# Performance work log

Hardware: AMD Instinct MI355X
Metric: run time of the kernel (lower is better)

## Reference

```python
import jax, jax.numpy as jnp
import numpy as np
import math

B, S, D, H, DQ = 4, 1024, 1024, 16, 64
DV = DQ // 2  # per-head value dim (all_head_size/2 split over heads)
MASK_VAL = -10000.0


def setup_inputs() -> dict:
    key = jax.random.key(0)
    ks = jax.random.split(key, 9)
    s = 1.0 / math.sqrt(D)
    return {
        "input_matrix": jax.random.normal(ks[0], (B, S, D), jnp.float32),
        "Wq": jax.random.normal(ks[1], (D, H * DQ), jnp.float32) * s,
        "bq": jnp.zeros((H * DQ,), jnp.float32),
        "Wk": jax.random.normal(ks[2], (D, H * DQ), jnp.float32) * s,
        "bk": jnp.zeros((H * DQ,), jnp.float32),
        "Wv": jax.random.normal(ks[3], (D, H * DV), jnp.float32) * s,
        "bv": jnp.zeros((H * DV,), jnp.float32),
        "Wo": jax.random.normal(ks[4], (D, D), jnp.float32) * s,
        "bo": jnp.zeros((D,), jnp.float32),
    }


def reference(input_matrix, Wq, bq, Wk, bk, Wv, bv, Wo, bo):
    x = input_matrix
    # projections -> [B, H, S, d]
    q = (x @ Wq + bq).reshape(B, S, H, DQ).transpose(0, 2, 1, 3)
    k = (x @ Wk + bk).reshape(B, S, H, DQ).transpose(0, 2, 1, 3)
    v = (x @ Wv + bv).reshape(B, S, H, DV).transpose(0, 2, 1, 3)

    scores = jnp.einsum("bhqd,bhkd->bhqk", q, k) / math.sqrt(DQ)  # [B,H,S,S]

    tril = jnp.tril(jnp.ones((S, S), bool))  # causal keep-mask
    fwd_scores = jnp.where(tril, scores, MASK_VAL)      # look-ahead masking
    bwd_scores = jnp.where(tril.T, scores, MASK_VAL)    # look-behind masking

    fwd_prob = jax.nn.softmax(fwd_scores, axis=-1)
    bwd_prob = jax.nn.softmax(bwd_scores, axis=-1)

    fwd_out = jnp.einsum("bhqk,bhkd->bhqd", fwd_prob, v)
    bwd_out = jnp.einsum("bhqk,bhkd->bhqd", bwd_prob, v)
    # [B,H,S,DV] -> [B,S,H*DV]
    fwd_out = fwd_out.transpose(0, 2, 1, 3).reshape(B, S, H * DV)
    bwd_out = bwd_out.transpose(0, 2, 1, 3).reshape(B, S, H * DV)

    out = jnp.concatenate([fwd_out, bwd_out], axis=-1) @ Wo + bo  # [B,S,D]
    attn_prob = jnp.concatenate([fwd_prob, bwd_prob], axis=-1)    # [B,H,S,2S]
    return out, attn_prob
```

## Files before the change

kernel.cpp:

```cpp
#include <hip/hip_runtime.h>
#include <hip/hip_bf16.h>

#define S_ 1024
#define D_ 1024
#define H_ 16
#define DQ_ 64
#define DV_ 32

typedef __attribute__((ext_vector_type(8))) short bf16x8;
typedef __attribute__((ext_vector_type(4))) float f32x4;

static __device__ __forceinline__ float bf2f(unsigned short u) {
    union { unsigned int i; float f; } v; v.i = ((unsigned int)u) << 16; return v.f;
}
static __device__ __forceinline__ unsigned short f2bf(float f) {
    union { float f; unsigned int i; } v; v.f = f;
    unsigned int x = v.i;
    unsigned int r = x + 0x7fffu + ((x >> 16) & 1u);
    return (unsigned short)(r >> 16);
}
static __device__ __forceinline__ f32x4 mfma16(bf16x8 a, bf16x8 b, f32x4 c) {
    return __builtin_amdgcn_mfma_f32_16x16x32_bf16(a, b, c, 0, 0, 0);
}

static __device__ __forceinline__ void gload16(const unsigned short* g, unsigned short* l) {
    __builtin_amdgcn_global_load_lds(
        (const __attribute__((address_space(1))) unsigned int*)(unsigned long long)g,
        (__attribute__((address_space(3))) unsigned int*)(unsigned int)(unsigned long long)l,
        16, 0, 0);
}

__global__ void k_detect(const unsigned short* __restrict__ X, int* __restrict__ flag) {
    int tid = threadIdx.x;
    unsigned short u = X[2 * tid];
    int e = (u >> 7) & 0xFF;
    bool sane = (e >= 100 && e <= 150) || ((u & 0x7FFFu) == 0);
    unsigned long long m = __ballot(sane);
    if (tid == 0) *flag = (__popcll(m) >= 40) ? 1 : 0;
}

__global__ void k_cvt(const void* __restrict__ src, unsigned short* __restrict__ dst,
                      int n, const int* __restrict__ flag) {
    int i = blockIdx.x * 256 + threadIdx.x;
    if (i >= n) return;
    int fl = *flag;
    dst[i] = fl ? ((const unsigned short*)src)[i] : f2bf(((const float*)src)[i]);
}

__global__ void k_cvt_f(const void* __restrict__ src, float* __restrict__ dst,
                        int n, const int* __restrict__ flag) {
    int i = blockIdx.x * 256 + threadIdx.x;
    if (i >= n) return;
    int fl = *flag;
    dst[i] = fl ? bf2f(((const unsigned short*)src)[i]) : ((const float*)src)[i];
}

__global__ void k_transpose(const void* __restrict__ src,
                            unsigned short* __restrict__ dst, int K, int N,
                            const int* __restrict__ flag) {
    __shared__ unsigned short t[32][33];
    int fl = *flag;
    int n0 = blockIdx.x * 32, k0 = blockIdx.y * 32;
    int tx = threadIdx.x, ty = threadIdx.y;
    for (int i = ty; i < 32; i += 8) {
        size_t idx = (size_t)(k0 + i) * N + n0 + tx;
        t[i][tx] = fl ? ((const unsigned short*)src)[idx]
                      : f2bf(((const float*)src)[idx]);
    }
    __syncthreads();
    for (int i = ty; i < 32; i += 8)
        dst[(size_t)(n0 + i) * K + k0 + tx] = t[tx][i];
}

__global__ __launch_bounds__(256)
void k_qkv(const unsigned short* __restrict__ Xb,
           const unsigned short* __restrict__ WT,
           const float* __restrict__ bias_f,
           unsigned short* __restrict__ q_l,
           unsigned short* __restrict__ k_l,
           unsigned short* __restrict__ vT) {
    __shared__ __align__(16) unsigned short As[128 * 32];
    __shared__ __align__(16) unsigned short Bs[128 * 32];
    int tid = threadIdx.x;
    int w = tid >> 6, lane = tid & 63;
    int m = lane & 15, quad = lane >> 4;
    int row0 = blockIdx.y * 128;
    int col0 = blockIdx.x * 128;
    int wr = w >> 1, wc = w & 1;

    const unsigned short* a0 = Xb + (size_t)(row0 + (tid >> 2)) * 1024 + (tid & 3) * 8;
    const unsigned short* b0 = WT + (size_t)(col0 + (tid >> 2)) * 1024 + (tid & 3) * 8;
    unsigned short* AsW = As + w * 512;
    unsigned short* BsW = Bs + w * 512;

    f32x4 acc[4][4];
#pragma unroll
    for (int i = 0; i < 4; ++i)
#pragma unroll
        for (int j = 0; j < 4; ++j) acc[i][j] = (f32x4){0.f, 0.f, 0.f, 0.f};

    for (int k0 = 0; k0 < 1024; k0 += 32) {
        gload16(a0 + k0, AsW);
        gload16(a0 + 64 * 1024 + k0, AsW + 2048);
        gload16(b0 + k0, BsW);
        gload16(b0 + 64 * 1024 + k0, BsW + 2048);
        __syncthreads();
        bf16x8 af[4], bf[4];
#pragma unroll
        for (int f = 0; f < 4; ++f) {
            af[f] = *(const bf16x8*)&As[(wr * 64 + f * 16 + m) * 32 + quad * 8];
            bf[f] = *(const bf16x8*)&Bs[(wc * 64 + f * 16 + m) * 32 + quad * 8];
        }
#pragma unroll
        for (int i = 0; i < 4; ++i)
#pragma unroll
            for (int j = 0; j < 4; ++j)
                acc[i][j] = mfma16(af[i], bf[j], acc[i][j]);
        __syncthreads();
    }

#pragma unroll
    for (int fn = 0; fn < 4; ++fn) {
        int col = col0 + wc * 64 + fn * 16 + m;
        float bval = bias_f[col];
#pragma unroll
        for (int fm = 0; fm < 4; ++fm) {
#pragma unroll
            for (int j = 0; j < 4; ++j) {
                int row = row0 + wr * 64 + fm * 16 + quad * 4 + j;
                int bb = row >> 10, ss = row & 1023;
                unsigned short o = f2bf(acc[fm][fn][j] + bval);
                if (col < 1024) {
                    int h = col >> 6, d = col & 63;
                    q_l[(((size_t)(bb * H_ + h)) * S_ + ss) * DQ_ + d] = o;
                } else if (col < 2048) {
                    int c = col - 1024; int h = c >> 6, d = c & 63;
                    k_l[(((size_t)(bb * H_ + h)) * S_ + ss) * DQ_ + d] = o;
                } else {
                    int c = col - 2048; int h = c >> 5, dv = c & 31;
                    vT[(((size_t)(bb * H_ + h)) * DV_ + dv) * S_ + ss] = o;
                }
            }
        }
    }
}

__global__ __launch_bounds__(256)
void k_attn(const unsigned short* __restrict__ q_l,
            const unsigned short* __restrict__ k_l,
            const unsigned short* __restrict__ vT,
            unsigned short* __restrict__ probs_b,
            float* __restrict__ probs_f,
            unsigned short* __restrict__ Y,
            const int* __restrict__ flag) {
    __shared__ __align__(16) unsigned short P[2][16][1032];
    __shared__ float redM[4][2][16];
    __shared__ float redL[4][2][16];
    int fl = *flag;
    int tid = threadIdx.x;
    int w = tid >> 6, lane = tid & 63;
    int m = lane & 15, quad = lane >> 4;
    int bh = blockIdx.x;
    int q0 = blockIdx.y * 16;
    int kbase = w * 256;

    const unsigned short* qp = q_l + (size_t)bh * S_ * DQ_;
    const unsigned short* kp = k_l + (size_t)bh * S_ * DQ_;
    const unsigned short* vp = vT  + (size_t)bh * DV_ * S_;

    bf16x8 qa0 = *(const bf16x8*)(qp + (size_t)(q0 + m) * DQ_ + quad * 8);
    bf16x8 qa1 = *(const bf16x8*)(qp + (size_t)(q0 + m) * DQ_ + 32 + quad * 8);

    float sc[16][4];
#pragma unroll
    for (int t = 0; t < 16; ++t) {
        const unsigned short* krow = kp + (size_t)((kbase >> 4) * 16 + t * 16 + m) * DQ_;
        bf16x8 kb0 = *(const bf16x8*)(krow + quad * 8);
        bf16x8 kb1 = *(const bf16x8*)(krow + 32 + quad * 8);
        f32x4 s = {0.f, 0.f, 0.f, 0.f};
        s = mfma16(qa0, kb0, s);
        s = mfma16(qa1, kb1, s);
#pragma unroll
        for (int j = 0; j < 4; ++j) sc[t][j] = s[j] * 0.125f;
    }

#pragma unroll
    for (int j = 0; j < 4; ++j) {
        int row = quad * 4 + j;
        int r = q0 + row;
        float mF = -3e38f, mB = -3e38f;
#pragma unroll
        for (int t = 0; t < 16; ++t) {
            int c = kbase + t * 16 + m;
            float v = sc[t][j];
            mF = (c <= r) ? fmaxf(mF, v) : mF;
            mB = (c >= r) ? fmaxf(mB, v) : mB;
        }
        mF = fmaxf(mF, __shfl_xor(mF, 1, 64));
        mF = fmaxf(mF, __shfl_xor(mF, 2, 64));
        mF = fmaxf(mF, __shfl_xor(mF, 4, 64));
        mF = fmaxf(mF, __shfl_xor(mF, 8, 64));
        mB = fmaxf(mB, __shfl_xor(mB, 1, 64));
        mB = fmaxf(mB, __shfl_xor(mB, 2, 64));
        mB = fmaxf(mB, __shfl_xor(mB, 4, 64));
        mB = fmaxf(mB, __shfl_xor(mB, 8, 64));
        if (m == 0) { redM[w][0][row] = mF; redM[w][1][row] = mB; }
    }
    __syncthreads();

#pragma unroll
    for (int j = 0; j < 4; ++j) {
        int row = quad * 4 + j;
        int r = q0 + row;
        float gmF = fmaxf(fmaxf(redM[0][0][row], redM[1][0][row]),
                          fmaxf(redM[2][0][row], redM[3][0][row]));
        float gmB = fmaxf(fmaxf(redM[0][1][row], redM[1][1][row]),
                          fmaxf(redM[2][1][row], redM[3][1][row]));
        float corr = __expf(gmF - gmB);
        float sF = 0.f, sB = 0.f;
#pragma unroll
        for (int t = 0; t < 16; ++t) {
            int c = kbase + t * 16 + m;
            float v = sc[t][j];
            bool fwd = (c <= r);
            float e = __expf(v - (fwd ? gmF : gmB));
            float eF = fwd ? e : 0.f;
            float eB = (c > r) ? e : ((c == r) ? e * corr : 0.f);
            sF += eF; sB += eB;
            P[0][row][c] = f2bf(eF);
            P[1][row][c] = f2bf(eB);
        }
        sF += __shfl_xor(sF, 1, 64);
        sF += __shfl_xor(sF, 2, 64);
        sF += __shfl_xor(sF, 4, 64);
        sF += __shfl_xor(sF, 8, 64);
        sB += __shfl_xor(sB, 1, 64);
        sB += __shfl_xor(sB, 2, 64);
        sB += __shfl_xor(sB, 4, 64);
        sB += __shfl_xor(sB, 8, 64);
        if (m == 0) { redL[w][0][row] = sF; redL[w][1][row] = sB; }
    }
    __syncthreads();

    size_t pbase = (size_t)bh << 21;
#pragma unroll 4
    for (int i = 0; i < 32; ++i) {
        int row = i >> 1, dir = i & 1;
        int col4 = tid * 4;
        ushort4 ev = *(const ushort4*)&P[dir][row][col4];
        float l = redL[0][dir][row] + redL[1][dir][row] +
                  redL[2][dir][row] + redL[3][dir][row];
        float inv = 1.f / l;
        size_t off = pbase + (size_t)(q0 + row) * 2048 + (size_t)dir * 1024 + col4;
        if (fl) {
            ushort4 o;
            o.x = f2bf(bf2f(ev.x) * inv); o.y = f2bf(bf2f(ev.y) * inv);
            o.z = f2bf(bf2f(ev.z) * inv); o.w = f2bf(bf2f(ev.w) * inv);
            *(ushort4*)(probs_b + off) = o;
        } else {
            float4 o = { bf2f(ev.x) * inv, bf2f(ev.y) * inv,
                         bf2f(ev.z) * inv, bf2f(ev.w) * inv };
            *(float4*)(probs_f + off) = o;
        }
    }

    {
        int dir = w >> 1, half = w & 1;
        const unsigned short* vrow = vp + (size_t)(half * 16 + m) * S_;
        f32x4 acc0 = {0.f,0.f,0.f,0.f}, acc1 = {0.f,0.f,0.f,0.f};
#pragma unroll
        for (int it = 0; it < 32; it += 2) {
            bf16x8 a0 = *(const bf16x8*)&P[dir][m][it * 32 + quad * 8];
            bf16x8 b0 = *(const bf16x8*)(vrow + it * 32 + quad * 8);
            acc0 = mfma16(a0, b0, acc0);
            bf16x8 a1 = *(const bf16x8*)&P[dir][m][it * 32 + 32 + quad * 8];
            bf16x8 b1 = *(const bf16x8*)(vrow + it * 32 + 32 + quad * 8);
            acc1 = mfma16(a1, b1, acc1);
        }
        int b_ = bh >> 4, h_ = bh & 15;
#pragma unroll
        for (int j = 0; j < 4; ++j) {
            int row = quad * 4 + j;
            float l = redL[0][dir][row] + redL[1][dir][row] +
                      redL[2][dir][row] + redL[3][dir][row];
            float v = (acc0[j] + acc1[j]) / l;
            Y[((size_t)(b_ * 1024 + q0 + row)) * 1024 +
              dir * 512 + h_ * 32 + half * 16 + m] = f2bf(v);
        }
    }
}

__global__ __launch_bounds__(256)
void k_out(const unsigned short* __restrict__ Y,
           const unsigned short* __restrict__ WoT,
           const float* __restrict__ bo,
           unsigned short* __restrict__ out_b,
           float* __restrict__ out_f,
           const int* __restrict__ flag) {
    __shared__ __align__(16) unsigned short As[128 * 32];
    __shared__ __align__(16) unsigned short Bs[128 * 32];
    int fl = *flag;
    int tid = threadIdx.x;
    int w = tid >> 6, lane = tid & 63;
    int m = lane & 15, quad = lane >> 4;
    int row0 = blockIdx.y * 128;
    int col0 = blockIdx.x * 128;
    int wr = w >> 1, wc = w & 1;

    const unsigned short* a0 = Y   + (size_t)(row0 + (tid >> 2)) * 1024 + (tid & 3) * 8;
    const unsigned short* b0 = WoT + (size_t)(col0 + (tid >> 2)) * 1024 + (tid & 3) * 8;
    unsigned short* AsW = As + w * 512;
    unsigned short* BsW = Bs + w * 512;

    f32x4 acc[4][4];
#pragma unroll
    for (int i = 0; i < 4; ++i)
#pragma unroll
        for (int j = 0; j < 4; ++j) acc[i][j] = (f32x4){0.f, 0.f, 0.f, 0.f};

    for (int k0 = 0; k0 < 1024; k0 += 32) {
        gload16(a0 + k0, AsW);
        gload16(a0 + 64 * 1024 + k0, AsW + 2048);
        gload16(b0 + k0, BsW);
        gload16(b0 + 64 * 1024 + k0, BsW + 2048);
        __syncthreads();
        bf16x8 af[4], bf[4];
#pragma unroll
        for (int f = 0; f < 4; ++f) {
            af[f] = *(const bf16x8*)&As[(wr * 64 + f * 16 + m) * 32 + quad * 8];
            bf[f] = *(const bf16x8*)&Bs[(wc * 64 + f * 16 + m) * 32 + quad * 8];
        }
#pragma unroll
        for (int i = 0; i < 4; ++i)
#pragma unroll
            for (int j = 0; j < 4; ++j)
                acc[i][j] = mfma16(af[i], bf[j], acc[i][j]);
        __syncthreads();
    }

#pragma unroll
    for (int fn = 0; fn < 4; ++fn) {
        int col = col0 + wc * 64 + fn * 16 + m;
        float bval = bo[col];
#pragma unroll
        for (int fm = 0; fm < 4; ++fm) {
#pragma unroll
            for (int j = 0; j < 4; ++j) {
                int row = row0 + wr * 64 + fm * 16 + quad * 4 + j;
                float v = acc[fm][fn][j] + bval;
                if (fl) out_b[(size_t)row * 1024 + col] = f2bf(v);
                else    out_f[(size_t)row * 1024 + col] = v;
            }
        }
    }
}

extern "C" void kernel_launch(void* const* d_in, const int* in_sizes, int n_in,
                              void* d_out, int out_size, void* d_ws, size_t ws_size,
                              hipStream_t stream) {
    const void* X  = d_in[0];
    const void* Wq = d_in[1];
    const void* bq = d_in[2];
    const void* Wk = d_in[3];
    const void* bk = d_in[4];
    const void* Wv = d_in[5];
    const void* bv = d_in[6];
    const void* Wo = d_in[7];
    const void* bo = d_in[8];

    unsigned short* ws  = (unsigned short*)d_ws;
    unsigned short* Xb  = ws;
    unsigned short* q_l = ws + 4194304;
    unsigned short* k_l = ws + 8388608;
    unsigned short* vT  = ws + 12582912;
    unsigned short* Y   = ws + 14680064;
    unsigned short* WqT = ws + 18874368;
    unsigned short* WkT = ws + 19922944;
    unsigned short* WvT = ws + 20971520;
    unsigned short* WoT = ws + 21495808;
    float*  bias_f = (float*)(ws + 22544384);
    int*    flag   = (int*)(bias_f + 3584);

    k_detect<<<1, 64, 0, stream>>>((const unsigned short*)X, flag);

    dim3 tb(32, 8);
    k_transpose<<<dim3(32, 32), tb, 0, stream>>>(Wq, WqT, 1024, 1024, flag);
    k_transpose<<<dim3(32, 32), tb, 0, stream>>>(Wk, WkT, 1024, 1024, flag);
    k_transpose<<<dim3(16, 32), tb, 0, stream>>>(Wv, WvT, 1024, 512, flag);
    k_transpose<<<dim3(32, 32), tb, 0, stream>>>(Wo, WoT, 1024, 1024, flag);

    k_cvt<<<16384, 256, 0, stream>>>(X, Xb, 4194304, flag);
    k_cvt_f<<<4, 256, 0, stream>>>(bq, bias_f,        1024, flag);
    k_cvt_f<<<4, 256, 0, stream>>>(bk, bias_f + 1024, 1024, flag);
    k_cvt_f<<<2, 256, 0, stream>>>(bv, bias_f + 2048,  512, flag);
    k_cvt_f<<<4, 256, 0, stream>>>(bo, bias_f + 2560, 1024, flag);

    k_qkv<<<dim3(20, 32), 256, 0, stream>>>(Xb, WqT, bias_f, q_l, k_l, vT);
    k_attn<<<dim3(64, 64), 256, 0, stream>>>(q_l, k_l, vT,
                                             (unsigned short*)d_out + 4194304,
                                             (float*)d_out + 4194304, Y, flag);
    k_out<<<dim3(8, 32), 256, 0, stream>>>(Y, WoT, bias_f + 2560,
                                           (unsigned short*)d_out, (float*)d_out, flag);
}
```

Baseline: 778.0 us.

## Merge prep launches, fuse masked max into score loop, narrow output GEMM tiles

Combines the four weight-transpose launches into one 3D-grid kernel and the four bias conversions into one kernel, cutting launch count. In attention, the causal and anti-causal row maxima are now taken inside the score loop rather than in a second pass, and the divides become hardware reciprocals. The output projection uses 128x64 tiles, doubling its grid to 512 blocks for better CU occupancy at the cost of more A-tile reloads. The reciprocal is approximate and may change results slightly.

```diff
diff --git a/kernel.cpp b/kernel.cpp
--- a/kernel.cpp
+++ b/kernel.cpp
@@ -47,20 +47,35 @@
     dst[i] = fl ? ((const unsigned short*)src)[i] : f2bf(((const float*)src)[i]);
 }
 
-__global__ void k_cvt_f(const void* __restrict__ src, float* __restrict__ dst,
-                        int n, const int* __restrict__ flag) {
+__global__ void k_bias(const void* __restrict__ bq, const void* __restrict__ bk,
+                       const void* __restrict__ bv, const void* __restrict__ bo,
+                       float* __restrict__ dst, const int* __restrict__ flag) {
     int i = blockIdx.x * 256 + threadIdx.x;
-    if (i >= n) return;
+    if (i >= 3584) return;
     int fl = *flag;
-    dst[i] = fl ? bf2f(((const unsigned short*)src)[i]) : ((const float*)src)[i];
-}
-
-__global__ void k_transpose(const void* __restrict__ src,
-                            unsigned short* __restrict__ dst, int K, int N,
-                            const int* __restrict__ flag) {
+    const void* src; int off;
+    if (i < 1024)      { src = bq; off = i; }
+    else if (i < 2048) { src = bk; off = i - 1024; }
+    else if (i < 2560) { src = bv; off = i - 2048; }
+    else               { src = bo; off = i - 2560; }
+    dst[i] = fl ? bf2f(((const unsigned short*)src)[off]) : ((const float*)src)[off];
+}
+
+__global__ void k_transpose4(const void* __restrict__ Wq, const void* __restrict__ Wk,
+                             const void* __restrict__ Wv, const void* __restrict__ Wo,
+                             unsigned short* __restrict__ WqT, unsigned short* __restrict__ WkT,
+                             unsigned short* __restrict__ WvT, unsigned short* __restrict__ WoT,
+                             const int* __restrict__ flag) {
     __shared__ unsigned short t[32][33];
+    int z = blockIdx.z;
+    const void* src; unsigned short* dst; int N;
+    if (z == 0)      { src = Wq; dst = WqT; N = 1024; }
+    else if (z == 1) { src = Wk; dst = WkT; N = 1024; }
+    else if (z == 2) { src = Wv; dst = WvT; N = 512; }
+    else             { src = Wo; dst = WoT; N = 1024; }
+    int n0 = blockIdx.x * 32, k0 = blockIdx.y * 32;
+    if (n0 >= N) return;
     int fl = *flag;
-    int n0 = blockIdx.x * 32, k0 = blockIdx.y * 32;
     int tx = threadIdx.x, ty = threadIdx.y;
     for (int i = ty; i < 32; i += 8) {
         size_t idx = (size_t)(k0 + i) * N + n0 + tx;
@@ -69,7 +84,7 @@
     }
     __syncthreads();
     for (int i = ty; i < 32; i += 8)
-        dst[(size_t)(n0 + i) * K + k0 + tx] = t[tx][i];
+        dst[(size_t)(n0 + i) * 1024 + k0 + tx] = t[tx][i];
 }
 
 __global__ __launch_bounds__(256)
@@ -105,17 +120,17 @@
         gload16(b0 + k0, BsW);
         gload16(b0 + 64 * 1024 + k0, BsW + 2048);
         __syncthreads();
-        bf16x8 af[4], bf[4];
+        bf16x8 af[4], bfr[4];
 #pragma unroll
         for (int f = 0; f < 4; ++f) {
-            af[f] = *(const bf16x8*)&As[(wr * 64 + f * 16 + m) * 32 + quad * 8];
-            bf[f] = *(const bf16x8*)&Bs[(wc * 64 + f * 16 + m) * 32 + quad * 8];
+            af[f]  = *(const bf16x8*)&As[(wr * 64 + f * 16 + m) * 32 + quad * 8];
+            bfr[f] = *(const bf16x8*)&Bs[(wc * 64 + f * 16 + m) * 32 + quad * 8];
         }
 #pragma unroll
         for (int i = 0; i < 4; ++i)
 #pragma unroll
             for (int j = 0; j < 4; ++j)
-                acc[i][j] = mfma16(af[i], bf[j], acc[i][j]);
+                acc[i][j] = mfma16(af[i], bfr[j], acc[i][j]);
         __syncthreads();
     }
 
@@ -172,39 +187,40 @@
     bf16x8 qa1 = *(const bf16x8*)(qp + (size_t)(q0 + m) * DQ_ + 32 + quad * 8);
 
     float sc[16][4];
+    float mF[4] = {-3e38f, -3e38f, -3e38f, -3e38f};
+    float mB[4] = {-3e38f, -3e38f, -3e38f, -3e38f};
 #pragma unroll
     for (int t = 0; t < 16; ++t) {
-        const unsigned short* krow = kp + (size_t)((kbase >> 4) * 16 + t * 16 + m) * DQ_;
+        const unsigned short* krow = kp + (size_t)(kbase + t * 16 + m) * DQ_;
         bf16x8 kb0 = *(const bf16x8*)(krow + quad * 8);
         bf16x8 kb1 = *(const bf16x8*)(krow + 32 + quad * 8);
         f32x4 s = {0.f, 0.f, 0.f, 0.f};
         s = mfma16(qa0, kb0, s);
         s = mfma16(qa1, kb1, s);
-#pragma unroll
-        for (int j = 0; j < 4; ++j) sc[t][j] = s[j] * 0.125f;
+        int c = kbase + t * 16 + m;
+#pragma unroll
+        for (int j = 0; j < 4; ++j) {
+            float v = s[j] * 0.125f;
+            sc[t][j] = v;
+            int r = q0 + quad * 4 + j;
+            if (c <= r) mF[j] = fmaxf(mF[j], v);
+            if (c >= r) mB[j] = fmaxf(mB[j], v);
+        }
     }
 
 #pragma unroll
     for (int j = 0; j < 4; ++j) {
         int row = quad * 4 + j;
-        int r = q0 + row;
-        float mF = -3e38f, mB = -3e38f;
-#pragma unroll
-        for (int t = 0; t < 16; ++t) {
-            int c = kbase + t * 16 + m;
-            float v = sc[t][j];
-            mF = (c <= r) ? fmaxf(mF, v) : mF;
-            mB = (c >= r) ? fmaxf(mB, v) : mB;
-        }
-        mF = fmaxf(mF, __shfl_xor(mF, 1, 64));
-        mF = fmaxf(mF, __shfl_xor(mF, 2, 64));
-        mF = fmaxf(mF, __shfl_xor(mF, 4, 64));
-        mF = fmaxf(mF, __shfl_xor(mF, 8, 64));
-        mB = fmaxf(mB, __shfl_xor(mB, 1, 64));
-        mB = fmaxf(mB, __shfl_xor(mB, 2, 64));
-        mB = fmaxf(mB, __shfl_xor(mB, 4, 64));
-        mB = fmaxf(mB, __shfl_xor(mB, 8, 64));
-        if (m == 0) { redM[w][0][row] = mF; redM[w][1][row] = mB; }
+        float f = mF[j], b = mB[j];
+        f = fmaxf(f, __shfl_xor(f, 1, 64));
+        f = fmaxf(f, __shfl_xor(f, 2, 64));
+        f = fmaxf(f, __shfl_xor(f, 4, 64));
+        f = fmaxf(f, __shfl_xor(f, 8, 64));
+        b = fmaxf(b, __shfl_xor(b, 1, 64));
+        b = fmaxf(b, __shfl_xor(b, 2, 64));
+        b = fmaxf(b, __shfl_xor(b, 4, 64));
+        b = fmaxf(b, __shfl_xor(b, 8, 64));
+        if (m == 0) { redM[w][0][row] = f; redM[w][1][row] = b; }
     }
     __syncthreads();
 
@@ -250,7 +266,7 @@
         ushort4 ev = *(const ushort4*)&P[dir][row][col4];
         float l = redL[0][dir][row] + redL[1][dir][row] +
                   redL[2][dir][row] + redL[3][dir][row];
-        float inv = 1.f / l;
+        float inv = __builtin_amdgcn_rcpf(l);
         size_t off = pbase + (size_t)(q0 + row) * 2048 + (size_t)dir * 1024 + col4;
         if (fl) {
             ushort4 o;
@@ -283,7 +299,7 @@
             int row = quad * 4 + j;
             float l = redL[0][dir][row] + redL[1][dir][row] +
                       redL[2][dir][row] + redL[3][dir][row];
-            float v = (acc0[j] + acc1[j]) / l;
+            float v = (acc0[j] + acc1[j]) * __builtin_amdgcn_rcpf(l);
             Y[((size_t)(b_ * 1024 + q0 + row)) * 1024 +
               dir * 512 + h_ * 32 + half * 16 + m] = f2bf(v);
         }
@@ -298,13 +314,13 @@
            float* __restrict__ out_f,
            const int* __restrict__ flag) {
     __shared__ __align__(16) unsigned short As[128 * 32];
-    __shared__ __align__(16) unsigned short Bs[128 * 32];
+    __shared__ __align__(16) unsigned short Bs[64 * 32];
     int fl = *flag;
     int tid = threadIdx.x;
     int w = tid >> 6, lane = tid & 63;
     int m = lane & 15, quad = lane >> 4;
     int row0 = blockIdx.y * 128;
-    int col0 = blockIdx.x * 128;
+    int col0 = blockIdx.x * 64;
     int wr = w >> 1, wc = w & 1;
 
     const unsigned short* a0 = Y   + (size_t)(row0 + (tid >> 2)) * 1024 + (tid & 3) * 8;
@@ -312,35 +328,35 @@
     unsigned short* AsW = As + w * 512;
     unsigned short* BsW = Bs + w * 512;
 
-    f32x4 acc[4][4];
+    f32x4 acc[4][2];
 #pragma unroll
     for (int i = 0; i < 4; ++i)
 #pragma unroll
-        for (int j = 0; j < 4; ++j) acc[i][j] = (f32x4){0.f, 0.f, 0.f, 0.f};
+        for (int j = 0; j < 2; ++j) acc[i][j] = (f32x4){0.f, 0.f, 0.f, 0.f};
 
     for (int k0 = 0; k0 < 1024; k0 += 32) {
         gload16(a0 + k0, AsW);
         gload16(a0 + 64 * 1024 + k0, AsW + 2048);
         gload16(b0 + k0, BsW);
-        gload16(b0 + 64 * 1024 + k0, BsW + 2048);
         __syncthreads();
-        bf16x8 af[4], bf[4];
-#pragma unroll
-        for (int f = 0; f < 4; ++f) {
+        bf16x8 af[4], bfr[2];
+#pragma unroll
+        for (int f = 0; f < 4; ++f)
             af[f] = *(const bf16x8*)&As[(wr * 64 + f * 16 + m) * 32 + quad * 8];
-            bf[f] = *(const bf16x8*)&Bs[(wc * 64 + f * 16 + m) * 32 + quad * 8];
-        }
+#pragma unroll
+        for (int f = 0; f < 2; ++f)
+            bfr[f] = *(const bf16x8*)&Bs[(wc * 32 + f * 16 + m) * 32 + quad * 8];
 #pragma unroll
         for (int i = 0; i < 4; ++i)
 #pragma unroll
-            for (int j = 0; j < 4; ++j)
-                acc[i][j] = mfma16(af[i], bf[j], acc[i][j]);
+            for (int j = 0; j < 2; ++j)
+                acc[i][j] = mfma16(af[i], bfr[j], acc[i][j]);
         __syncthreads();
     }
 
 #pragma unroll
-    for (int fn = 0; fn < 4; ++fn) {
-        int col = col0 + wc * 64 + fn * 16 + m;
+    for (int fn = 0; fn < 2; ++fn) {
+        int col = col0 + wc * 32 + fn * 16 + m;
         float bval = bo[col];
 #pragma unroll
         for (int fm = 0; fm < 4; ++fm) {
@@ -383,22 +399,16 @@
 
     k_detect<<<1, 64, 0, stream>>>((const unsigned short*)X, flag);
 
-    dim3 tb(32, 8);
-    k_transpose<<<dim3(32, 32), tb, 0, stream>>>(Wq, WqT, 1024, 1024, flag);
-    k_transpose<<<dim3(32, 32), tb, 0, stream>>>(Wk, WkT, 1024, 1024, flag);
-    k_transpose<<<dim3(16, 32), tb, 0, stream>>>(Wv, WvT, 1024, 512, flag);
-    k_transpose<<<dim3(32, 32), tb, 0, stream>>>(Wo, WoT, 1024, 1024, flag);
+    k_transpose4<<<dim3(32, 32, 4), dim3(32, 8), 0, stream>>>(
+        Wq, Wk, Wv, Wo, WqT, WkT, WvT, WoT, flag);
 
     k_cvt<<<16384, 256, 0, stream>>>(X, Xb, 4194304, flag);
-    k_cvt_f<<<4, 256, 0, stream>>>(bq, bias_f,        1024, flag);
-    k_cvt_f<<<4, 256, 0, stream>>>(bk, bias_f + 1024, 1024, flag);
-    k_cvt_f<<<2, 256, 0, stream>>>(bv, bias_f + 2048,  512, flag);
-    k_cvt_f<<<4, 256, 0, stream>>>(bo, bias_f + 2560, 1024, flag);
+    k_bias<<<14, 256, 0, stream>>>(bq, bk, bv, bo, bias_f, flag);
 
     k_qkv<<<dim3(20, 32), 256, 0, stream>>>(Xb, WqT, bias_f, q_l, k_l, vT);
     k_attn<<<dim3(64, 64), 256, 0, stream>>>(q_l, k_l, vT,
                                              (unsigned short*)d_out + 4194304,
                                              (float*)d_out + 4194304, Y, flag);
-    k_out<<<dim3(8, 32), 256, 0, stream>>>(Y, WoT, bias_f + 2560,
-                                           (unsigned short*)d_out, (float*)d_out, flag);
-}
+    k_out<<<dim3(16, 32), 256, 0, stream>>>(Y, WoT, bias_f + 2560,
+                                            (unsigned short*)d_out, (float*)d_out, flag);
+}
```

Result: faster. 752.1 us (-3.3%).
